# Kernel optimization log

Measured on AMD Instinct MI355X. Metric: run time of the kernel, lower is better.

The kernel has to match this reference:

```python
import jax, jax.numpy as jnp
import numpy as np

EPS_LN = 1e-6
EPS_L2 = 1e-12

def _ln(x, g, b):
    m = jnp.mean(x, axis=-1, keepdims=True)
    v = jnp.mean((x - m) ** 2, axis=-1, keepdims=True)
    return (x - m) / jnp.sqrt(v + EPS_LN) * g + b

def _l2norm(x, axis):
    n = jnp.sqrt(jnp.sum(x * x, axis=axis, keepdims=True))
    return x / jnp.maximum(n, EPS_L2)

def setup_inputs() -> dict:
    key = jax.random.key(0)
    ks = jax.random.split(key, 5)
    b, h, w, d = 32, 64, 64, 192
    td, ad = 768, 128
    return dict(
        x=jax.random.normal(ks[0], (b, h, w, d), jnp.float32),
        token=jax.random.normal(ks[1], (b, td), jnp.float32),
        p=jax.random.uniform(ks[2], (b, 1), jnp.float32),
        alpha=jnp.zeros((1,), jnp.float32),
        ln1_g=jnp.ones((td,), jnp.float32), ln1_b=jnp.zeros((td,), jnp.float32),
        w_tok=jax.random.normal(ks[3], (td, ad), jnp.float32) * 0.02,
        b_tok=jnp.zeros((ad,), jnp.float32),
        ln2_g=jnp.ones((d,), jnp.float32), ln2_b=jnp.zeros((d,), jnp.float32),
        w_x=jax.random.normal(ks[4], (d, ad), jnp.float32) * 0.02,
        b_x=jnp.zeros((ad,), jnp.float32),
        ln3_g=jnp.ones((d,), jnp.float32), ln3_b=jnp.zeros((d,), jnp.float32),
    )

def reference(x, token, p, alpha, ln1_g, ln1_b, w_tok, b_tok, ln2_g, ln2_b, w_x, b_x, ln3_g, ln3_b):
    b, h, w, d = x.shape
    # token_proj(norm1(token)) : [b, attn_dims]
    tok = jax.nn.gelu(_ln(token, ln1_g, ln1_b) @ w_tok + b_tok, approximate=False)
    # x_proj(norm2(x flattened)) : [b, hw, attn_dims]
    xf = x.reshape(b, h * w, d)
    x_ = jax.nn.gelu(_ln(xf, ln2_g, ln2_b) @ w_x + b_x, approximate=False)
    # L2-normalized skinny dot-product attention -> [b, hw]
    xn = _l2norm(x_, axis=2)
    tn = _l2norm(tok, axis=1)
    attn = p * jnp.einsum('bnk,bk->bn', xn, tn) * jnp.exp(alpha)  # p:[b,1] broadcasts
    attn = attn.reshape(b, h, w)
    # residual: 0.5*x + norm3(x * attn)
    out = 0.5 * x + _ln(x * attn[..., None], ln3_g, ln3_b)
    return out
```

## Files before the change

### kernel.cpp

```cpp
#include <hip/hip_runtime.h>
#include <math.h>

typedef _Float16 f16;
typedef f16  v8h __attribute__((ext_vector_type(8)));
typedef float v4f __attribute__((ext_vector_type(4)));

#define EPS_LN 1e-6f
#define GELU_K 0.70710678118654752440f
#define LO_SCALE 65536.0f
#define LO_INV   (1.0f/65536.0f)

#define WS_TN 98304

__device__ __forceinline__ void split16(float v, f16& hi, f16& lo){
  hi = (f16)v;
  lo = (f16)((v - (float)hi) * LO_SCALE);
}

__global__ __launch_bounds__(64) void prep_w(const float* __restrict__ wx, uint4* __restrict__ wf){
  const int S = blockIdx.x >> 3, t = blockIdx.x & 7, l = threadIdx.x;
  const int n  = (t << 4) + (l & 15);
  const int k0 = (S << 5) + ((l >> 4) << 3);
  union { v8h v; uint4 u; } H, L;
  #pragma unroll
  for(int j = 0; j < 8; ++j){
    float v = wx[(size_t)(k0 + j)*128 + n];
    f16 h, lo; split16(v, h, lo);
    H.v[j] = h; L.v[j] = lo;
  }
  wf[(0*6 + S)*512 + t*64 + l] = H.u;
  wf[(1*6 + S)*512 + t*64 + l] = L.u;
}

__global__ __launch_bounds__(256) void tok_kernel(
    const float* __restrict__ token, const float* __restrict__ p, const float* __restrict__ alpha,
    const float* __restrict__ g1, const float* __restrict__ b1,
    const float* __restrict__ w_tok, const float* __restrict__ b_tok,
    float* __restrict__ tn_out)
{
  __shared__ float ln[768];
  __shared__ float part[256];
  __shared__ float yv[128];
  __shared__ float rs1[4], rs2[4];
  const int b = blockIdx.x;
  const int t = threadIdx.x;
  const int lane = t & 63, wid = t >> 6;
  const float* tok = token + b*768;

  float v0 = tok[t], v1 = tok[t+256], v2 = tok[t+512];
  float s1 = v0+v1+v2, s2 = v0*v0+v1*v1+v2*v2;
  #pragma unroll
  for(int m = 1; m < 64; m <<= 1){ s1 += __shfl_xor(s1,m,64); s2 += __shfl_xor(s2,m,64); }
  if(lane == 0){ rs1[wid] = s1; rs2[wid] = s2; }
  __syncthreads();
  float S1 = rs1[0]+rs1[1]+rs1[2]+rs1[3];
  float S2 = rs2[0]+rs2[1]+rs2[2]+rs2[3];
  float mean = S1*(1.f/768.f);
  float var  = S2*(1.f/768.f) - mean*mean;
  float rstd = rsqrtf(var + EPS_LN);
  ln[t]       = (v0-mean)*rstd*g1[t]       + b1[t];
  ln[t + 256] = (v1-mean)*rstd*g1[t + 256] + b1[t + 256];
  ln[t + 512] = (v2-mean)*rstd*g1[t + 512] + b1[t + 512];
  __syncthreads();

  const int k  = t & 127;
  const int d0 = (t >> 7) * 384;
  float acc = 0.f;
  for(int d = 0; d < 384; ++d)
    acc = fmaf(ln[d0 + d], w_tok[(size_t)(d0 + d)*128 + k], acc);
  part[t] = acc;
  __syncthreads();
  if(t < 128){
    float y = part[t] + part[t + 128] + b_tok[k];
    y = 0.5f*y*(1.f + erff(y*GELU_K));
    yv[t] = y;
  }
  __syncthreads();
  float ss = (t < 128) ? yv[t]*yv[t] : 0.f;
  #pragma unroll
  for(int m = 1; m < 64; m <<= 1) ss += __shfl_xor(ss, m, 64);
  if(lane == 0) rs1[wid] = ss;
  __syncthreads();
  float SS = rs1[0]+rs1[1]+rs1[2]+rs1[3];
  float scale = p[b]*expf(alpha[0]) / fmaxf(sqrtf(SS), 1e-12f);
  if(t < 128) tn_out[b*128 + t] = yv[t]*scale;
}

__global__ __launch_bounds__(256, 2) void x_kernel(
    const float* __restrict__ x, const float* __restrict__ g2, const float* __restrict__ b2,
    const uint4* __restrict__ wf, const float* __restrict__ bx,
    const float* __restrict__ g3, const float* __restrict__ b3,
    const float* __restrict__ tn, float* __restrict__ out)
{
  __shared__ f16   llds[2*64*104];
  __shared__ float attn_sm[64];

  const int t = threadIdx.x, lane = t & 63, wv = t >> 6;
  const int q = lane & 3, r = lane >> 2;
  const size_t row0 = (size_t)blockIdx.x * 64;
  const int bidx = (int)(row0 >> 12);
  const float* xrow = x + (row0 + wv*16 + r)*192 + q*48;

  float xv[48];
  #pragma unroll
  for(int i = 0; i < 12; ++i) *(float4*)&xv[i*4] = *(const float4*)(xrow + i*4);
  float s1 = 0.f, s2 = 0.f;
  #pragma unroll
  for(int i = 0; i < 48; ++i){ s1 += xv[i]; s2 = fmaf(xv[i], xv[i], s2); }
  s1 += __shfl_xor(s1, 1, 64); s1 += __shfl_xor(s1, 2, 64);
  s2 += __shfl_xor(s2, 1, 64); s2 += __shfl_xor(s2, 2, 64);
  const float mu   = s1 * (1.f/192.f);
  const float var  = s2 * (1.f/192.f) - mu*mu;
  const float rstd = rsqrtf(var + EPS_LN);

  auto write_ln = [&](int half){
    if((q >> 1) == half){
      const float* g2p = g2 + q*48;
      const float* b2p = b2 + q*48;
      const int base = (wv*16 + r)*104 + (q & 1)*48;
      #pragma unroll
      for(int i = 0; i < 48; i += 8){
        union { v8h v; uint4 u; } H, L;
        #pragma unroll
        for(int j = 0; j < 8; ++j){
          float lv = (xv[i+j] - mu)*rstd*g2p[i+j] + b2p[i+j];
          f16 h, lo; split16(lv, h, lo);
          H.v[j] = h; L.v[j] = lo;
        }
        *(uint4*)&llds[       base + i] = H.u;
        *(uint4*)&llds[6656 + base + i] = L.u;
      }
    }
  };

  v4f C1[8], C2[8];
  #pragma unroll
  for(int tt = 0; tt < 8; ++tt){ C1[tt] = (v4f){0.f,0.f,0.f,0.f}; C2[tt] = (v4f){0.f,0.f,0.f,0.f}; }

  auto do_mfma = [&](int half){
    #pragma unroll
    for(int s = 0; s < 3; ++s){
      const int abase = (wv*16 + (lane & 15))*104 + ((lane >> 4) << 3) + s*32;
      v8h ah = *(v8h*)&llds[abase];
      v8h al = *(v8h*)&llds[6656 + abase];
      const int S = half*3 + s;
      #pragma unroll
      for(int tt = 0; tt < 8; ++tt){
        v8h bh = *(const v8h*)&wf[(0*6 + S)*512 + tt*64 + lane];
        v8h bl = *(const v8h*)&wf[(1*6 + S)*512 + tt*64 + lane];
        C1[tt] = __builtin_amdgcn_mfma_f32_16x16x32_f16(ah, bh, C1[tt], 0, 0, 0);
        C2[tt] = __builtin_amdgcn_mfma_f32_16x16x32_f16(al, bh, C2[tt], 0, 0, 0);
        C2[tt] = __builtin_amdgcn_mfma_f32_16x16x32_f16(ah, bl, C2[tt], 0, 0, 0);
      }
    }
  };

  write_ln(0);
  __syncthreads();
  do_mfma(0);
  __syncthreads();
  write_ln(1);
  __syncthreads();
  do_mfma(1);

  const float* tnb = tn + bidx*128;
  const int n0 = lane & 15;
  float ss[4] = {0,0,0,0}, dt[4] = {0,0,0,0};
  #pragma unroll
  for(int tt = 0; tt < 8; ++tt){
    const int col = n0 + 16*tt;
    const float bxv = bx[col], tnv = tnb[col];
    #pragma unroll
    for(int g = 0; g < 4; ++g){
      float y = fmaf(C2[tt][g], LO_INV, C1[tt][g]) + bxv;
      y = 0.5f*y*(1.f + erff(y*GELU_K));
      ss[g] = fmaf(y, y,   ss[g]);
      dt[g] = fmaf(y, tnv, dt[g]);
    }
  }
  #pragma unroll
  for(int g = 0; g < 4; ++g){
    #pragma unroll
    for(int m = 1; m < 16; m <<= 1){ ss[g] += __shfl_xor(ss[g], m, 64); dt[g] += __shfl_xor(dt[g], m, 64); }
  }
  if(n0 == 0){
    const int quad = lane >> 4;
    #pragma unroll
    for(int g = 0; g < 4; ++g)
      attn_sm[wv*16 + quad*4 + g] = dt[g] / fmaxf(sqrtf(ss[g]), 1e-12f);
  }
  __syncthreads();
  const float attn = attn_sm[wv*16 + r];

  const float rd = rsqrtf(attn*attn*var + EPS_LN);
  const float am = attn * rd;
  const float* g3p = g3 + q*48;
  const float* b3p = b3 + q*48;
  float* orow = out + (row0 + wv*16 + r)*192 + q*48;
  #pragma unroll
  for(int i = 0; i < 12; ++i){
    float4 gv = *(const float4*)(g3p + i*4);
    float4 bv = *(const float4*)(b3p + i*4);
    float4 o;
    o.x = fmaf(0.5f, xv[i*4+0], fmaf(am*(xv[i*4+0]-mu), gv.x, bv.x));
    o.y = fmaf(0.5f, xv[i*4+1], fmaf(am*(xv[i*4+1]-mu), gv.y, bv.y));
    o.z = fmaf(0.5f, xv[i*4+2], fmaf(am*(xv[i*4+2]-mu), gv.z, bv.z));
    o.w = fmaf(0.5f, xv[i*4+3], fmaf(am*(xv[i*4+3]-mu), gv.w, bv.w));
    *(float4*)(orow + i*4) = o;
  }
}

extern "C" void kernel_launch(void* const* d_in, const int* in_sizes, int n_in,
                              void* d_out, int out_size, void* d_ws, size_t ws_size,
                              hipStream_t stream) {
  const float* x     = (const float*)d_in[0];
  const float* token = (const float*)d_in[1];
  const float* p     = (const float*)d_in[2];
  const float* alpha = (const float*)d_in[3];
  const float* g1    = (const float*)d_in[4];
  const float* b1    = (const float*)d_in[5];
  const float* wtok  = (const float*)d_in[6];
  const float* btok  = (const float*)d_in[7];
  const float* g2    = (const float*)d_in[8];
  const float* b2    = (const float*)d_in[9];
  const float* wx    = (const float*)d_in[10];
  const float* bx    = (const float*)d_in[11];
  const float* g3    = (const float*)d_in[12];
  const float* b3    = (const float*)d_in[13];

  uint4* wf = (uint4*)d_ws;
  float* tn = (float*)((char*)d_ws + WS_TN);
  float* outf = (float*)d_out;

  prep_w<<<48, 64, 0, stream>>>(wx, wf);
  tok_kernel<<<32, 256, 0, stream>>>(token, p, alpha, g1, b1, wtok, btok, tn);
  x_kernel<<<2048, 256, 0, stream>>>(x, g2, b2, wf, bx, g3, b3, tn, outf);
}
```

Before: 313.1 us.

## Keep weight fragments in registers and split MFMA output columns across waves

New measurement: 267.7 us. 14.5% less time.

```diff
diff --git a/kernel.cpp b/kernel.cpp
--- a/kernel.cpp
+++ b/kernel.cpp
@@ -11,6 +11,9 @@
 #define LO_INV   (1.0f/65536.0f)
 
 #define WS_TN 98304
+
+#define LSTR 216
+#define KOFF (64*216)
 
 __device__ __forceinline__ void split16(float v, f16& hi, f16& lo){
   hi = (f16)v;
@@ -65,10 +68,16 @@
 
   const int k  = t & 127;
   const int d0 = (t >> 7) * 384;
-  float acc = 0.f;
-  for(int d = 0; d < 384; ++d)
-    acc = fmaf(ln[d0 + d], w_tok[(size_t)(d0 + d)*128 + k], acc);
-  part[t] = acc;
+  const float* wp = w_tok + (size_t)d0*128 + k;
+  float a0 = 0.f, a1 = 0.f, a2 = 0.f, a3 = 0.f;
+  #pragma unroll 4
+  for(int d = 0; d < 384; d += 4){
+    a0 = fmaf(ln[d0+d+0], wp[(size_t)(d+0)*128], a0);
+    a1 = fmaf(ln[d0+d+1], wp[(size_t)(d+1)*128], a1);
+    a2 = fmaf(ln[d0+d+2], wp[(size_t)(d+2)*128], a2);
+    a3 = fmaf(ln[d0+d+3], wp[(size_t)(d+3)*128], a3);
+  }
+  part[t] = (a0+a1)+(a2+a3);
   __syncthreads();
   if(t < 128){
     float y = part[t] + part[t + 128] + b_tok[k];
@@ -92,14 +101,25 @@
     const float* __restrict__ g3, const float* __restrict__ b3,
     const float* __restrict__ tn, float* __restrict__ out)
 {
-  __shared__ f16   llds[2*64*104];
-  __shared__ float attn_sm[64];
+  __shared__ f16   llds[2*64*LSTR];
+  __shared__ float pss[4][64], pdt[4][64];
 
   const int t = threadIdx.x, lane = t & 63, wv = t >> 6;
   const int q = lane & 3, r = lane >> 2;
   const size_t row0 = (size_t)blockIdx.x * 64;
   const int bidx = (int)(row0 >> 12);
-  const float* xrow = x + (row0 + wv*16 + r)*192 + q*48;
+  const int myrow = wv*16 + r;
+  const float* xrow = x + (row0 + myrow)*192 + q*48;
+
+  v8h Bh[6][2], Bl[6][2];
+  #pragma unroll
+  for(int S = 0; S < 6; ++S){
+    #pragma unroll
+    for(int u = 0; u < 2; ++u){
+      Bh[S][u] = *(const v8h*)&wf[(0*6 + S)*512 + (2*wv + u)*64 + lane];
+      Bl[S][u] = *(const v8h*)&wf[(1*6 + S)*512 + (2*wv + u)*64 + lane];
+    }
+  }
 
   float xv[48];
   #pragma unroll
@@ -113,90 +133,83 @@
   const float var  = s2 * (1.f/192.f) - mu*mu;
   const float rstd = rsqrtf(var + EPS_LN);
 
-  auto write_ln = [&](int half){
-    if((q >> 1) == half){
-      const float* g2p = g2 + q*48;
-      const float* b2p = b2 + q*48;
-      const int base = (wv*16 + r)*104 + (q & 1)*48;
-      #pragma unroll
-      for(int i = 0; i < 48; i += 8){
-        union { v8h v; uint4 u; } H, L;
-        #pragma unroll
-        for(int j = 0; j < 8; ++j){
-          float lv = (xv[i+j] - mu)*rstd*g2p[i+j] + b2p[i+j];
-          f16 h, lo; split16(lv, h, lo);
-          H.v[j] = h; L.v[j] = lo;
-        }
-        *(uint4*)&llds[       base + i] = H.u;
-        *(uint4*)&llds[6656 + base + i] = L.u;
-      }
-    }
-  };
-
-  v4f C1[8], C2[8];
-  #pragma unroll
-  for(int tt = 0; tt < 8; ++tt){ C1[tt] = (v4f){0.f,0.f,0.f,0.f}; C2[tt] = (v4f){0.f,0.f,0.f,0.f}; }
-
-  auto do_mfma = [&](int half){
-    #pragma unroll
-    for(int s = 0; s < 3; ++s){
-      const int abase = (wv*16 + (lane & 15))*104 + ((lane >> 4) << 3) + s*32;
-      v8h ah = *(v8h*)&llds[abase];
-      v8h al = *(v8h*)&llds[6656 + abase];
-      const int S = half*3 + s;
-      #pragma unroll
-      for(int tt = 0; tt < 8; ++tt){
-        v8h bh = *(const v8h*)&wf[(0*6 + S)*512 + tt*64 + lane];
-        v8h bl = *(const v8h*)&wf[(1*6 + S)*512 + tt*64 + lane];
-        C1[tt] = __builtin_amdgcn_mfma_f32_16x16x32_f16(ah, bh, C1[tt], 0, 0, 0);
-        C2[tt] = __builtin_amdgcn_mfma_f32_16x16x32_f16(al, bh, C2[tt], 0, 0, 0);
-        C2[tt] = __builtin_amdgcn_mfma_f32_16x16x32_f16(ah, bl, C2[tt], 0, 0, 0);
-      }
-    }
-  };
-
-  write_ln(0);
-  __syncthreads();
-  do_mfma(0);
-  __syncthreads();
-  write_ln(1);
-  __syncthreads();
-  do_mfma(1);
-
+  {
+    const float* g2p = g2 + q*48;
+    const float* b2p = b2 + q*48;
+    const int base = myrow*LSTR + q*48;
+    #pragma unroll
+    for(int i = 0; i < 48; i += 8){
+      union { v8h v; uint4 u; } H, L;
+      #pragma unroll
+      for(int j = 0; j < 8; ++j){
+        float lv = (xv[i+j] - mu)*rstd*g2p[i+j] + b2p[i+j];
+        f16 h, lo; split16(lv, h, lo);
+        H.v[j] = h; L.v[j] = lo;
+      }
+      *(uint4*)&llds[       base + i] = H.u;
+      *(uint4*)&llds[KOFF + base + i] = L.u;
+    }
+  }
+  __syncthreads();
+
+  const int n0 = lane & 15, quad = lane >> 4;
   const float* tnb = tn + bidx*128;
-  const int n0 = lane & 15;
-  float ss[4] = {0,0,0,0}, dt[4] = {0,0,0,0};
-  #pragma unroll
-  for(int tt = 0; tt < 8; ++tt){
-    const int col = n0 + 16*tt;
-    const float bxv = bx[col], tnv = tnb[col];
+  #pragma unroll
+  for(int mt = 0; mt < 4; ++mt){
+    v4f c1[2], c2[2];
+    #pragma unroll
+    for(int u = 0; u < 2; ++u){ c1[u] = (v4f){0,0,0,0}; c2[u] = (v4f){0,0,0,0}; }
+    #pragma unroll
+    for(int S = 0; S < 6; ++S){
+      const int ab = (mt*16 + n0)*LSTR + quad*8 + S*32;
+      v8h ah = *(v8h*)&llds[ab];
+      v8h al = *(v8h*)&llds[KOFF + ab];
+      #pragma unroll
+      for(int u = 0; u < 2; ++u){
+        c1[u] = __builtin_amdgcn_mfma_f32_16x16x32_f16(ah, Bh[S][u], c1[u], 0, 0, 0);
+        c2[u] = __builtin_amdgcn_mfma_f32_16x16x32_f16(al, Bh[S][u], c2[u], 0, 0, 0);
+        c2[u] = __builtin_amdgcn_mfma_f32_16x16x32_f16(ah, Bl[S][u], c2[u], 0, 0, 0);
+      }
+    }
+    float ssv[4] = {0,0,0,0}, dtv[4] = {0,0,0,0};
+    #pragma unroll
+    for(int u = 0; u < 2; ++u){
+      const int col = n0 + 16*(2*wv + u);
+      const float bxv = bx[col], tnv = tnb[col];
+      #pragma unroll
+      for(int g = 0; g < 4; ++g){
+        float y = fmaf(c2[u][g], LO_INV, c1[u][g]) + bxv;
+        y = 0.5f*y*(1.f + erff(y*GELU_K));
+        ssv[g] = fmaf(y, y,   ssv[g]);
+        dtv[g] = fmaf(y, tnv, dtv[g]);
+      }
+    }
     #pragma unroll
     for(int g = 0; g < 4; ++g){
-      float y = fmaf(C2[tt][g], LO_INV, C1[tt][g]) + bxv;
-      y = 0.5f*y*(1.f + erff(y*GELU_K));
-      ss[g] = fmaf(y, y,   ss[g]);
-      dt[g] = fmaf(y, tnv, dt[g]);
-    }
-  }
-  #pragma unroll
-  for(int g = 0; g < 4; ++g){
-    #pragma unroll
-    for(int m = 1; m < 16; m <<= 1){ ss[g] += __shfl_xor(ss[g], m, 64); dt[g] += __shfl_xor(dt[g], m, 64); }
-  }
-  if(n0 == 0){
-    const int quad = lane >> 4;
-    #pragma unroll
-    for(int g = 0; g < 4; ++g)
-      attn_sm[wv*16 + quad*4 + g] = dt[g] / fmaxf(sqrtf(ss[g]), 1e-12f);
-  }
-  __syncthreads();
-  const float attn = attn_sm[wv*16 + r];
-
+      #pragma unroll
+      for(int m = 1; m < 16; m <<= 1){
+        ssv[g] += __shfl_xor(ssv[g], m, 64);
+        dtv[g] += __shfl_xor(dtv[g], m, 64);
+      }
+    }
+    if(n0 == 0){
+      #pragma unroll
+      for(int g = 0; g < 4; ++g){
+        pss[wv][mt*16 + quad*4 + g] = ssv[g];
+        pdt[wv][mt*16 + quad*4 + g] = dtv[g];
+      }
+    }
+  }
+  __syncthreads();
+
+  const float SSt = pss[0][myrow] + pss[1][myrow] + pss[2][myrow] + pss[3][myrow];
+  const float DTt = pdt[0][myrow] + pdt[1][myrow] + pdt[2][myrow] + pdt[3][myrow];
+  const float attn = DTt / fmaxf(sqrtf(SSt), 1e-12f);
   const float rd = rsqrtf(attn*attn*var + EPS_LN);
   const float am = attn * rd;
   const float* g3p = g3 + q*48;
   const float* b3p = b3 + q*48;
-  float* orow = out + (row0 + wv*16 + r)*192 + q*48;
+  float* orow = out + (row0 + myrow)*192 + q*48;
   #pragma unroll
   for(int i = 0; i < 12; ++i){
     float4 gv = *(const float4*)(g3p + i*4);
```
